# Kernel tuning notes

Measured on AMD Instinct MI355X. Metric: run time of the kernel, lower is better.

## Reference

```python
import jax, jax.numpy as jnp
import numpy as np

D_MODEL = 1024
NUM_HEADS = 16
D_HEAD = D_MODEL // NUM_HEADS
B, T = 2, 2048


def setup_inputs() -> dict:
    key = jax.random.key(0)
    kx, kq, kk, kv, ko = jax.random.split(key, 5)
    # xavier_uniform bound for square (D,D) linear weights
    bound = float(np.sqrt(6.0 / (D_MODEL + D_MODEL)))
    uni = lambda k: jax.random.uniform(k, (D_MODEL, D_MODEL), jnp.float32, -bound, bound)
    return {
        "x": jax.random.normal(kx, (B, T, D_MODEL), jnp.float32),
        "Wq": uni(kq),
        "Wk": uni(kk),
        "Wv": uni(kv),
        "Wo": uni(ko),
    }


def _split_heads(x):
    # (B, T, D) -> (B, H, T, d_head)
    b, t, _ = x.shape
    return x.reshape(b, t, NUM_HEADS, D_HEAD).transpose(0, 2, 1, 3)


def _exclusive_output_mod(Y, V):
    dt = V.dtype
    tiny = jnp.asarray(jnp.finfo(dt).tiny, dt)
    eps = jnp.asarray(jnp.finfo(dt).eps, dt)
    v_sq = jnp.sum(V * V, axis=-1, keepdims=True)
    y_dot_v = jnp.sum(Y * V, axis=-1, keepdims=True)
    scale = jnp.where(v_sq > 0, y_dot_v / jnp.maximum(v_sq, tiny), jnp.zeros_like(y_dot_v))
    Z = Y - scale * V
    residual_norm = jnp.linalg.norm(Z, axis=-1, keepdims=True)
    reference_norm = jnp.maximum(
        jnp.linalg.norm(Y, axis=-1, keepdims=True),
        jnp.linalg.norm(V, axis=-1, keepdims=True),
    )
    cleanup_tol = eps * Z.shape[-1] * reference_norm
    return jnp.where((v_sq > 0) & (residual_norm <= cleanup_tol), jnp.zeros_like(Z), Z)


def reference(x, Wq, Wk, Wv, Wo):
    Q = _split_heads(x @ Wq.T)  # (B,H,T,dh)
    K = _split_heads(x @ Wk.T)
    V = _split_heads(x @ Wv.T)
    sm_scale = 1.0 / np.sqrt(D_HEAD)
    scores = jnp.einsum("bhqd,bhkd->bhqk", Q, K) * sm_scale
    P = jax.nn.softmax(scores, axis=-1)
    Y = jnp.einsum("bhqk,bhkd->bhqd", P, V)
    Z = _exclusive_output_mod(Y, V)
    # merge heads: (B,H,T,dh) -> (B,T,D)
    Zm = Z.transpose(0, 2, 1, 3).reshape(x.shape[0], x.shape[1], D_MODEL)
    return Zm @ Wo.T
```

## Files before the change

### kernel.cpp

```cpp
#include <hip/hip_runtime.h>
#include <math.h>

#define DM   1024
#define TTOK 2048
#define NTOK 4096

typedef __bf16 bf16x8 __attribute__((ext_vector_type(8)));
typedef __bf16 bf16x4 __attribute__((ext_vector_type(4)));
typedef float  f32x4  __attribute__((ext_vector_type(4)));
typedef float  f32x16 __attribute__((ext_vector_type(16)));

#define QSCALE 0.18033688011112042f

#if defined(__has_builtin)
#if __has_builtin(__builtin_amdgcn_exp2f)
#define EXP2F(x) __builtin_amdgcn_exp2f(x)
#endif
#endif
#ifndef EXP2F
#define EXP2F(x) exp2f(x)
#endif

#define GLDS16(g, l) __builtin_amdgcn_global_load_lds( \
    (__attribute__((address_space(1))) void*)(g),      \
    (__attribute__((address_space(3))) void*)(l), 16, 0, 0)

__global__ __launch_bounds__(256)
void cvt_all(const float* __restrict__ x,  const float* __restrict__ Wq,
             const float* __restrict__ Wk, const float* __restrict__ Wv,
             const float* __restrict__ Wo, __bf16* __restrict__ dst) {
    size_t g = ((size_t)blockIdx.x * 256 + threadIdx.x) * 8;
    const float* s;
    size_t off;
    const size_t NX = (size_t)NTOK * DM;
    if (g < NX) { s = x; off = g; }
    else {
        size_t gg = g - NX;
        int w = (int)(gg >> 20);
        off = gg & ((1u << 20) - 1);
        s = (w == 0) ? Wq : (w == 1) ? Wk : (w == 2) ? Wv : Wo;
    }
    float4 a = *(const float4*)(s + off);
    float4 b = *(const float4*)(s + off + 4);
    bf16x8 v;
    v[0] = (__bf16)a.x; v[1] = (__bf16)a.y; v[2] = (__bf16)a.z; v[3] = (__bf16)a.w;
    v[4] = (__bf16)b.x; v[5] = (__bf16)b.y; v[6] = (__bf16)b.z; v[7] = (__bf16)b.w;
    *(bf16x8*)(dst + g) = v;
}

#define LSTR 136

template<int MODE>
__global__ __launch_bounds__(256)
void gemm_bf16(const __bf16* __restrict__ X,
               const __bf16* __restrict__ W0, const __bf16* __restrict__ W1,
               const __bf16* __restrict__ W2,
               __bf16* __restrict__ Oq, __bf16* __restrict__ Ok,
               __bf16* __restrict__ Ovt, float* __restrict__ Of)
{
    const int z = (MODE == 0) ? blockIdx.z : 3;
    const __bf16 *A, *B;
    int m0, n0;
    if (MODE == 0 && z < 2) {
        A = z ? W1 : W0; B = X;
        m0 = blockIdx.y * 128; n0 = blockIdx.x * 128;
    } else if (MODE == 0) {
        A = X; B = W2;
        m0 = blockIdx.x * 128; n0 = blockIdx.y * 128;
    } else {
        A = X; B = W0;
        m0 = blockIdx.y * 128; n0 = blockIdx.x * 128;
    }

    __shared__ __attribute__((aligned(16))) __bf16 smem[128 * LSTR];
    __bf16* As = smem;
    __bf16* Bs = smem + 128 * 32;

    const int tid  = threadIdx.x;
    const int lane = tid & 63;
    const int wave = tid >> 6;
    const int wm = wave & 1, wn = wave >> 1;
    const int col = lane & 15, quad = lane >> 4;

    const __bf16* Ag = A + (size_t)(m0 + (tid >> 2)) * DM + (tid & 3) * 8;
    const __bf16* Bg = B + (size_t)(n0 + (tid >> 2)) * DM + (tid & 3) * 8;
    __bf16* lA = As + tid * 8;
    __bf16* lB = Bs + tid * 8;

    f32x4 acc[4][4];
#pragma unroll
    for (int i = 0; i < 4; ++i)
#pragma unroll
        for (int j = 0; j < 4; ++j)
#pragma unroll
            for (int r = 0; r < 4; ++r) acc[i][j][r] = 0.0f;

    for (int k0 = 0; k0 < DM; k0 += 32) {
        __syncthreads();
        GLDS16(Ag + k0,                   lA);
        GLDS16(Ag + (size_t)64 * DM + k0, lA + 2048);
        GLDS16(Bg + k0,                   lB);
        GLDS16(Bg + (size_t)64 * DM + k0, lB + 2048);
        __syncthreads();
        bf16x8 af[4], bfr[4];
#pragma unroll
        for (int i = 0; i < 4; ++i)
            af[i] = *(const bf16x8*)&As[(wm * 64 + i * 16 + col) * 32 + quad * 8];
#pragma unroll
        for (int j = 0; j < 4; ++j)
            bfr[j] = *(const bf16x8*)&Bs[(wn * 64 + j * 16 + col) * 32 + quad * 8];
#pragma unroll
        for (int i = 0; i < 4; ++i)
#pragma unroll
            for (int j = 0; j < 4; ++j)
                acc[i][j] = __builtin_amdgcn_mfma_f32_16x16x32_bf16(af[i], bfr[j], acc[i][j], 0, 0, 0);
    }

    if (MODE == 1) {
#pragma unroll
        for (int i = 0; i < 4; ++i)
#pragma unroll
            for (int j = 0; j < 4; ++j) {
                const int mb = m0 + wm * 64 + i * 16 + quad * 4;
                const int n  = n0 + wn * 64 + j * 16 + col;
#pragma unroll
                for (int r = 0; r < 4; ++r)
                    Of[(size_t)(mb + r) * DM + n] = acc[i][j][r];
            }
        return;
    }

    const float sc = (z == 0) ? QSCALE : 1.0f;
    __syncthreads();
#pragma unroll
    for (int i = 0; i < 4; ++i)
#pragma unroll
        for (int j = 0; j < 4; ++j) {
            const int ml = wm * 64 + i * 16 + quad * 4;
            const int nl = wn * 64 + j * 16 + col;
            bf16x4 pk;
#pragma unroll
            for (int r = 0; r < 4; ++r) pk[r] = (__bf16)(acc[i][j][r] * sc);
            *(bf16x4*)&smem[nl * LSTR + ml] = pk;
        }
    __syncthreads();

#pragma unroll
    for (int it = 0; it < 8; ++it) {
        int c   = tid + 256 * it;
        int row = c >> 4;
        int ch  = (c & 15) * 8;
        bf16x8 v = *(const bf16x8*)&smem[row * LSTR + ch];
        if (z < 2) {
            int t  = n0 + row;
            int b  = t >> 11; t &= 2047;
            int hd = m0 + ch;
            int h  = hd >> 6, d = hd & 63;
            *(bf16x8*)&((z ? Ok : Oq)[(((size_t)(b * 16 + h)) * TTOK + t) * 64 + d]) = v;
        } else {
            int hd = n0 + row;
            int h  = hd >> 6, d = hd & 63;
            int t  = m0 + ch;
            int b  = t >> 11; t &= 2047;
            *(bf16x8*)&Ovt[(((size_t)(b * 16 + h)) * 64 + d) * TTOK + t] = v;
        }
    }
}

__global__ __launch_bounds__(256)
void attn_mfma(const __bf16* __restrict__ Qg, const __bf16* __restrict__ Kg,
               const __bf16* __restrict__ Vtg, __bf16* __restrict__ Zm)
{
    const int bh = blockIdx.y;
    const int q0 = blockIdx.x * 128;
    const size_t base = (size_t)bh * TTOK * 64;

    __shared__ __attribute__((aligned(16))) __bf16 Ks[64 * 72];
    __shared__ __attribute__((aligned(16))) __bf16 Vs[64 * 72];
    __shared__ __attribute__((aligned(16))) __bf16 QPs[128 * 72];

    const int tid  = threadIdx.x;
    const int lane = tid & 63, wave = tid >> 6;
    const int c32  = lane & 31, h32 = lane >> 5;

#pragma unroll
    for (int it = 0; it < 2; ++it) {
        int idx = tid + 256 * it;
        int r = idx >> 2, off = (idx & 3) * 16;
        const __bf16* src = Qg + base + (size_t)(q0 + r) * 64 + off;
        *(bf16x8*)&QPs[r * 72 + off]     = *(const bf16x8*)(src);
        *(bf16x8*)&QPs[r * 72 + off + 8] = *(const bf16x8*)(src + 8);
    }
    __syncthreads();
    bf16x8 qf[4];
#pragma unroll
    for (int st = 0; st < 4; ++st)
        qf[st] = *(const bf16x8*)&QPs[(wave * 32 + c32) * 72 + h32 * 8 + st * 16];

    bf16x8 ones;
#pragma unroll
    for (int i = 0; i < 8; ++i) ones[i] = (__bf16)1.0f;

    f32x16 O[2], lacc;
#pragma unroll
    for (int r = 0; r < 16; ++r) { O[0][r] = 0.0f; O[1][r] = 0.0f; lacc[r] = 0.0f; }

    const int rs = tid >> 2, soff = (tid & 3) * 16;

    bf16x8 kr0 = *(const bf16x8*)(Kg  + base + (size_t)rs * 64 + soff);
    bf16x8 kr1 = *(const bf16x8*)(Kg  + base + (size_t)rs * 64 + soff + 8);
    bf16x8 vr0 = *(const bf16x8*)(Vtg + base + (size_t)rs * TTOK + soff);
    bf16x8 vr1 = *(const bf16x8*)(Vtg + base + (size_t)rs * TTOK + soff + 8);

    const int kb_tgt = (q0 >> 6) + (wave >> 1);
    const int qo     = (wave & 1) * 32 + c32;
    float vq[2][16];

    for (int kb = 0; kb < TTOK / 64; ++kb) {
        __syncthreads();
        *(bf16x8*)&Ks[rs * 72 + soff]     = kr0;
        *(bf16x8*)&Ks[rs * 72 + soff + 8] = kr1;
        *(bf16x8*)&Vs[rs * 72 + soff]     = vr0;
        *(bf16x8*)&Vs[rs * 72 + soff + 8] = vr1;
        __syncthreads();

        {
            int kbn = (kb + 1) & (TTOK / 64 - 1);
            const __bf16* kp = Kg  + base + (size_t)(kbn * 64 + rs) * 64 + soff;
            const __bf16* vp = Vtg + base + (size_t)rs * TTOK + kbn * 64 + soff;
            kr0 = *(const bf16x8*)(kp); kr1 = *(const bf16x8*)(kp + 8);
            vr0 = *(const bf16x8*)(vp); vr1 = *(const bf16x8*)(vp + 8);
        }

        f32x16 s0, s1;
#pragma unroll
        for (int r = 0; r < 16; ++r) { s0[r] = 0.0f; s1[r] = 0.0f; }
#pragma unroll
        for (int st = 0; st < 4; ++st) {
            bf16x8 a0 = *(const bf16x8*)&Ks[(c32)      * 72 + h32 * 8 + st * 16];
            bf16x8 a1 = *(const bf16x8*)&Ks[(32 + c32) * 72 + h32 * 8 + st * 16];
            s0 = __builtin_amdgcn_mfma_f32_32x32x16_bf16(a0, qf[st], s0, 0, 0, 0);
            s1 = __builtin_amdgcn_mfma_f32_32x32x16_bf16(a1, qf[st], s1, 0, 0, 0);
        }

#pragma unroll
        for (int kb2 = 0; kb2 < 2; ++kb2) {
#pragma unroll
            for (int g = 0; g < 4; ++g) {
                float p0 = EXP2F(kb2 ? s1[4 * g + 0] : s0[4 * g + 0]);
                float p1 = EXP2F(kb2 ? s1[4 * g + 1] : s0[4 * g + 1]);
                float p2 = EXP2F(kb2 ? s1[4 * g + 2] : s0[4 * g + 2]);
                float p3 = EXP2F(kb2 ? s1[4 * g + 3] : s0[4 * g + 3]);
                bf16x4 pk;
                pk[0] = (__bf16)p0; pk[1] = (__bf16)p1;
                pk[2] = (__bf16)p2; pk[3] = (__bf16)p3;
                *(bf16x4*)&QPs[(wave * 32 + c32) * 72 + kb2 * 32 + g * 8 + h32 * 4] = pk;
            }
        }

#pragma unroll
        for (int ks = 0; ks < 4; ++ks) {
            bf16x8 pf = *(const bf16x8*)&QPs[(wave * 32 + c32) * 72 + h32 * 8 + ks * 16];
            lacc = __builtin_amdgcn_mfma_f32_32x32x16_bf16(ones, pf, lacc, 0, 0, 0);
            bf16x8 v0 = *(const bf16x8*)&Vs[(c32)      * 72 + h32 * 8 + ks * 16];
            bf16x8 v1 = *(const bf16x8*)&Vs[(32 + c32) * 72 + h32 * 8 + ks * 16];
            O[0] = __builtin_amdgcn_mfma_f32_32x32x16_bf16(v0, pf, O[0], 0, 0, 0);
            O[1] = __builtin_amdgcn_mfma_f32_32x32x16_bf16(v1, pf, O[1], 0, 0, 0);
        }

        if (kb == kb_tgt) {
#pragma unroll
            for (int db = 0; db < 2; ++db)
#pragma unroll
                for (int rg = 0; rg < 16; ++rg) {
                    int d = db * 32 + (rg & 3) + 8 * (rg >> 2) + 4 * h32;
                    vq[db][rg] = (float)Vs[d * 72 + qo];
                }
        }
    }

    const float inv = 1.0f / lacc[0];

    const int b = bh >> 4, h = bh & 15;
    const int q = q0 + wave * 32 + c32;
    float y[2][16];
    float yv = 0.f, v2 = 0.f, yy = 0.f;
#pragma unroll
    for (int db = 0; db < 2; ++db)
#pragma unroll
        for (int rg = 0; rg < 16; ++rg) {
            float yval = O[db][rg] * inv;
            float vval = vq[db][rg];
            y[db][rg] = yval;
            yv += yval * vval; v2 += vval * vval; yy += yval * yval;
        }
    yv += __shfl_xor(yv, 32, 64);
    v2 += __shfl_xor(v2, 32, 64);
    yy += __shfl_xor(yy, 32, 64);
    float scl = (v2 > 0.0f) ? yv / fmaxf(v2, 1.1754943508222875e-38f) : 0.0f;
    float zz = 0.f;
    float zvv[2][16];
#pragma unroll
    for (int db = 0; db < 2; ++db)
#pragma unroll
        for (int rg = 0; rg < 16; ++rg) {
            zvv[db][rg] = y[db][rg] - scl * vq[db][rg];
            zz += zvv[db][rg] * zvv[db][rg];
        }
    zz += __shfl_xor(zz, 32, 64);
    float znorm = sqrtf(zz);
    float refn  = fmaxf(sqrtf(yy), sqrtf(v2));
    bool  wipe  = (v2 > 0.0f) && (znorm <= 1.1920928955078125e-07f * 64.0f * refn);
#pragma unroll
    for (int db = 0; db < 2; ++db)
#pragma unroll
        for (int g = 0; g < 4; ++g) {
            bf16x4 pk;
#pragma unroll
            for (int r = 0; r < 4; ++r)
                pk[r] = (__bf16)(wipe ? 0.0f : zvv[db][4 * g + r]);
            int d = db * 32 + 8 * g + 4 * h32;
            *(bf16x4*)&Zm[((size_t)(b * TTOK + q)) * DM + h * 64 + d] = pk;
        }
}

extern "C" void kernel_launch(void* const* d_in, const int* in_sizes, int n_in,
                              void* d_out, int out_size, void* d_ws, size_t ws_size,
                              hipStream_t stream) {
    const float* x  = (const float*)d_in[0];
    const float* Wq = (const float*)d_in[1];
    const float* Wk = (const float*)d_in[2];
    const float* Wv = (const float*)d_in[3];
    const float* Wo = (const float*)d_in[4];

    const size_t NX = (size_t)NTOK * DM;
    const size_t NW = (size_t)DM * DM;
    __bf16* xb  = (__bf16*)d_ws;
    __bf16* wqb = xb  + NX;
    __bf16* wkb = wqb + NW;
    __bf16* wvb = wkb + NW;
    __bf16* wob = wvb + NW;
    __bf16* Qb  = wob + NW;
    __bf16* Kb  = Qb  + NX;
    __bf16* Vtb = Kb  + NX;
    __bf16* Zmb = Vtb + NX;

    cvt_all<<<(NX + 4 * NW) / 2048, 256, 0, stream>>>(x, Wq, Wk, Wv, Wo, xb);

    gemm_bf16<0><<<dim3(32, 8, 3), 256, 0, stream>>>(
        xb, wqb, wkb, wvb, Qb, Kb, Vtb, nullptr);

    attn_mfma<<<dim3(TTOK / 128, 32), 256, 0, stream>>>(Qb, Kb, Vtb, Zmb);

    gemm_bf16<1><<<dim3(8, 32), 256, 0, stream>>>(
        Zmb, wob, nullptr, nullptr, nullptr, nullptr, nullptr, (float*)d_out);
}
```

Baseline: 190.2 us.

## Split attention KV range across waves and load K/V fragments directly from global

```diff
diff --git a/kernel.cpp b/kernel.cpp
--- a/kernel.cpp
+++ b/kernel.cpp
@@ -24,6 +24,8 @@
 #define GLDS16(g, l) __builtin_amdgcn_global_load_lds( \
     (__attribute__((address_space(1))) void*)(g),      \
     (__attribute__((address_space(3))) void*)(l), 16, 0, 0)
+
+#define MFMA32(a, b, c) __builtin_amdgcn_mfma_f32_32x32x16_bf16((a), (b), (c), 0, 0, 0)
 
 __global__ __launch_bounds__(256)
 void cvt_all(const float* __restrict__ x,  const float* __restrict__ Wq,
@@ -172,127 +174,138 @@
                const __bf16* __restrict__ Vtg, __bf16* __restrict__ Zm)
 {
     const int bh = blockIdx.y;
-    const int q0 = blockIdx.x * 128;
+    const int q0 = blockIdx.x * 64;
     const size_t base = (size_t)bh * TTOK * 64;
 
-    __shared__ __attribute__((aligned(16))) __bf16 Ks[64 * 72];
-    __shared__ __attribute__((aligned(16))) __bf16 Vs[64 * 72];
-    __shared__ __attribute__((aligned(16))) __bf16 QPs[128 * 72];
+    __shared__ float cbuf[2 * 33 * 64];
 
     const int tid  = threadIdx.x;
     const int lane = tid & 63, wave = tid >> 6;
     const int c32  = lane & 31, h32 = lane >> 5;
-
-#pragma unroll
-    for (int it = 0; it < 2; ++it) {
-        int idx = tid + 256 * it;
-        int r = idx >> 2, off = (idx & 3) * 16;
-        const __bf16* src = Qg + base + (size_t)(q0 + r) * 64 + off;
-        *(bf16x8*)&QPs[r * 72 + off]     = *(const bf16x8*)(src);
-        *(bf16x8*)&QPs[r * 72 + off + 8] = *(const bf16x8*)(src + 8);
+    const int qg   = wave & 1,  kh  = wave >> 1;
+    const int sigc = (c32 & 19) | ((c32 & 4) << 1) | ((c32 & 8) >> 1);
+    const int q    = q0 + qg * 32 + c32;
+    const int doff = h32 * 8;
+
+    bf16x8 qf[4];
+    {
+        const __bf16* qp = Qg + base + (size_t)q * 64 + doff;
+#pragma unroll
+        for (int st = 0; st < 4; ++st) qf[st] = *(const bf16x8*)(qp + st * 16);
+    }
+
+    f32x16 O0, O1;
+#pragma unroll
+    for (int r = 0; r < 16; ++r) { O0[r] = 0.0f; O1[r] = 0.0f; }
+    float lsum = 0.0f;
+
+    const int kb0 = kh * 16, kb1 = kb0 + 16;
+    const __bf16* kbase  = Kg  + base + (size_t)sigc * 64 + doff;
+    const __bf16* vbase0 = Vtg + base + (size_t)c32 * TTOK + doff;
+    const __bf16* vbase1 = Vtg + base + (size_t)(c32 + 32) * TTOK + doff;
+
+    bf16x8 kf0[4], kf1[4];
+    {
+        const __bf16* kp = kbase + (size_t)kb0 * 4096;
+#pragma unroll
+        for (int st = 0; st < 4; ++st) {
+            kf0[st] = *(const bf16x8*)(kp + st * 16);
+            kf1[st] = *(const bf16x8*)(kp + 2048 + st * 16);
+        }
+    }
+
+    for (int kb = kb0; kb < kb1; ++kb) {
+        f32x16 s0, s1;
+#pragma unroll
+        for (int r = 0; r < 16; ++r) { s0[r] = 0.0f; s1[r] = 0.0f; }
+#pragma unroll
+        for (int st = 0; st < 4; ++st) {
+            s0 = MFMA32(kf0[st], qf[st], s0);
+            s1 = MFMA32(kf1[st], qf[st], s1);
+        }
+
+        bf16x8 vf0[4], vf1[4];
+        {
+            const __bf16* vp0 = vbase0 + kb * 64;
+            const __bf16* vp1 = vbase1 + kb * 64;
+#pragma unroll
+            for (int st = 0; st < 4; ++st) {
+                vf0[st] = *(const bf16x8*)(vp0 + st * 16);
+                vf1[st] = *(const bf16x8*)(vp1 + st * 16);
+            }
+        }
+
+        bf16x8 pf[4];
+        float acc = 0.0f;
+#pragma unroll
+        for (int st = 0; st < 4; ++st) {
+            int b0 = (st & 1) * 8;
+#pragma unroll
+            for (int j = 0; j < 8; ++j) {
+                float p = EXP2F((st < 2) ? s0[b0 + j] : s1[b0 + j]);
+                acc += p;
+                pf[st][j] = (__bf16)p;
+            }
+        }
+        lsum += acc;
+
+#pragma unroll
+        for (int st = 0; st < 4; ++st) {
+            O0 = MFMA32(vf0[st], pf[st], O0);
+            O1 = MFMA32(vf1[st], pf[st], O1);
+        }
+
+        if (kb + 1 < kb1) {
+            const __bf16* kp = kbase + (size_t)(kb + 1) * 4096;
+#pragma unroll
+            for (int st = 0; st < 4; ++st) {
+                kf0[st] = *(const bf16x8*)(kp + st * 16);
+                kf1[st] = *(const bf16x8*)(kp + 2048 + st * 16);
+            }
+        }
+    }
+
+    lsum += __shfl_xor(lsum, 32, 64);
+
+    float* cb = cbuf + qg * 33 * 64;
+    if (kh == 1) {
+#pragma unroll
+        for (int r = 0; r < 16; ++r) {
+            cb[r * 64 + lane]        = O0[r];
+            cb[(16 + r) * 64 + lane] = O1[r];
+        }
+        cb[32 * 64 + lane] = lsum;
     }
     __syncthreads();
-    bf16x8 qf[4];
-#pragma unroll
-    for (int st = 0; st < 4; ++st)
-        qf[st] = *(const bf16x8*)&QPs[(wave * 32 + c32) * 72 + h32 * 8 + st * 16];
-
-    bf16x8 ones;
-#pragma unroll
-    for (int i = 0; i < 8; ++i) ones[i] = (__bf16)1.0f;
-
-    f32x16 O[2], lacc;
-#pragma unroll
-    for (int r = 0; r < 16; ++r) { O[0][r] = 0.0f; O[1][r] = 0.0f; lacc[r] = 0.0f; }
-
-    const int rs = tid >> 2, soff = (tid & 3) * 16;
-
-    bf16x8 kr0 = *(const bf16x8*)(Kg  + base + (size_t)rs * 64 + soff);
-    bf16x8 kr1 = *(const bf16x8*)(Kg  + base + (size_t)rs * 64 + soff + 8);
-    bf16x8 vr0 = *(const bf16x8*)(Vtg + base + (size_t)rs * TTOK + soff);
-    bf16x8 vr1 = *(const bf16x8*)(Vtg + base + (size_t)rs * TTOK + soff + 8);
-
-    const int kb_tgt = (q0 >> 6) + (wave >> 1);
-    const int qo     = (wave & 1) * 32 + c32;
-    float vq[2][16];
-
-    for (int kb = 0; kb < TTOK / 64; ++kb) {
-        __syncthreads();
-        *(bf16x8*)&Ks[rs * 72 + soff]     = kr0;
-        *(bf16x8*)&Ks[rs * 72 + soff + 8] = kr1;
-        *(bf16x8*)&Vs[rs * 72 + soff]     = vr0;
-        *(bf16x8*)&Vs[rs * 72 + soff + 8] = vr1;
-        __syncthreads();
-
-        {
-            int kbn = (kb + 1) & (TTOK / 64 - 1);
-            const __bf16* kp = Kg  + base + (size_t)(kbn * 64 + rs) * 64 + soff;
-            const __bf16* vp = Vtg + base + (size_t)rs * TTOK + kbn * 64 + soff;
-            kr0 = *(const bf16x8*)(kp); kr1 = *(const bf16x8*)(kp + 8);
-            vr0 = *(const bf16x8*)(vp); vr1 = *(const bf16x8*)(vp + 8);
-        }
-
-        f32x16 s0, s1;
-#pragma unroll
-        for (int r = 0; r < 16; ++r) { s0[r] = 0.0f; s1[r] = 0.0f; }
-#pragma unroll
-        for (int st = 0; st < 4; ++st) {
-            bf16x8 a0 = *(const bf16x8*)&Ks[(c32)      * 72 + h32 * 8 + st * 16];
-            bf16x8 a1 = *(const bf16x8*)&Ks[(32 + c32) * 72 + h32 * 8 + st * 16];
-            s0 = __builtin_amdgcn_mfma_f32_32x32x16_bf16(a0, qf[st], s0, 0, 0, 0);
-            s1 = __builtin_amdgcn_mfma_f32_32x32x16_bf16(a1, qf[st], s1, 0, 0, 0);
-        }
-
-#pragma unroll
-        for (int kb2 = 0; kb2 < 2; ++kb2) {
-#pragma unroll
-            for (int g = 0; g < 4; ++g) {
-                float p0 = EXP2F(kb2 ? s1[4 * g + 0] : s0[4 * g + 0]);
-                float p1 = EXP2F(kb2 ? s1[4 * g + 1] : s0[4 * g + 1]);
-                float p2 = EXP2F(kb2 ? s1[4 * g + 2] : s0[4 * g + 2]);
-                float p3 = EXP2F(kb2 ? s1[4 * g + 3] : s0[4 * g + 3]);
-                bf16x4 pk;
-                pk[0] = (__bf16)p0; pk[1] = (__bf16)p1;
-                pk[2] = (__bf16)p2; pk[3] = (__bf16)p3;
-                *(bf16x4*)&QPs[(wave * 32 + c32) * 72 + kb2 * 32 + g * 8 + h32 * 4] = pk;
-            }
-        }
-
-#pragma unroll
-        for (int ks = 0; ks < 4; ++ks) {
-            bf16x8 pf = *(const bf16x8*)&QPs[(wave * 32 + c32) * 72 + h32 * 8 + ks * 16];
-            lacc = __builtin_amdgcn_mfma_f32_32x32x16_bf16(ones, pf, lacc, 0, 0, 0);
-            bf16x8 v0 = *(const bf16x8*)&Vs[(c32)      * 72 + h32 * 8 + ks * 16];
-            bf16x8 v1 = *(const bf16x8*)&Vs[(32 + c32) * 72 + h32 * 8 + ks * 16];
-            O[0] = __builtin_amdgcn_mfma_f32_32x32x16_bf16(v0, pf, O[0], 0, 0, 0);
-            O[1] = __builtin_amdgcn_mfma_f32_32x32x16_bf16(v1, pf, O[1], 0, 0, 0);
-        }
-
-        if (kb == kb_tgt) {
-#pragma unroll
-            for (int db = 0; db < 2; ++db)
-#pragma unroll
-                for (int rg = 0; rg < 16; ++rg) {
-                    int d = db * 32 + (rg & 3) + 8 * (rg >> 2) + 4 * h32;
-                    vq[db][rg] = (float)Vs[d * 72 + qo];
-                }
-        }
-    }
-
-    const float inv = 1.0f / lacc[0];
+    if (kh == 1) return;
+#pragma unroll
+    for (int r = 0; r < 16; ++r) {
+        O0[r] += cb[r * 64 + lane];
+        O1[r] += cb[(16 + r) * 64 + lane];
+    }
+    lsum += cb[32 * 64 + lane];
+
+    const float inv = 1.0f / lsum;
 
     const int b = bh >> 4, h = bh & 15;
-    const int q = q0 + wave * 32 + c32;
-    float y[2][16];
+    float vq[2][16], y[2][16];
+#pragma unroll
+    for (int db = 0; db < 2; ++db)
+#pragma unroll
+        for (int rg = 0; rg < 16; ++rg) {
+            int d = db * 32 + (rg & 3) + 8 * (rg >> 2) + 4 * h32;
+            vq[db][rg] = (float)Vtg[base + (size_t)d * TTOK + q];
+        }
     float yv = 0.f, v2 = 0.f, yy = 0.f;
 #pragma unroll
     for (int db = 0; db < 2; ++db)
 #pragma unroll
         for (int rg = 0; rg < 16; ++rg) {
-            float yval = O[db][rg] * inv;
-            float vval = vq[db][rg];
+            float yval = (db ? O1[rg] : O0[rg]) * inv;
             y[db][rg] = yval;
-            yv += yval * vval; v2 += vval * vval; yy += yval * yval;
+            yv += yval * vq[db][rg];
+            v2 += vq[db][rg] * vq[db][rg];
+            yy += yval * yval;
         }
     yv += __shfl_xor(yv, 32, 64);
     v2 += __shfl_xor(v2, 32, 64);
@@ -350,7 +363,7 @@
     gemm_bf16<0><<<dim3(32, 8, 3), 256, 0, stream>>>(
         xb, wqb, wkb, wvb, Qb, Kb, Vtb, nullptr);
 
-    attn_mfma<<<dim3(TTOK / 128, 32), 256, 0, stream>>>(Qb, Kb, Vtb, Zmb);
+    attn_mfma<<<dim3(TTOK / 64, 32), 256, 0, stream>>>(Qb, Kb, Vtb, Zmb);
 
     gemm_bf16<1><<<dim3(8, 32), 256, 0, stream>>>(
         Zmb, wob, nullptr, nullptr, nullptr, nullptr, nullptr, (float*)d_out);
```

Result: slower. 257.3 us (+35.2%).
